# Kernel tuning notes

Hardware: AMD Instinct MI355X
Metric: run time of the kernel (lower is better)

Reference implementation:

```python
import jax, jax.numpy as jnp
import numpy as np


def setup_inputs() -> dict:
    key = jax.random.key(0)
    ks = jax.random.split(key, 6)
    B, Nab, Nag, d, K = 16, 16384, 16384, 128, 10
    return {
        "H1": jax.random.normal(ks[0], (B, Nab, d), jnp.float32),
        "H2": jax.random.normal(ks[1], (B, Nag, d), jnp.float32),
        "X1": jax.random.normal(ks[2], (B, Nab, 3), jnp.float32),
        "X2": jax.random.normal(ks[3], (B, Nag, 3), jnp.float32),
        "W1": jax.random.uniform(ks[4], (K, d, d), jnp.float32),
        "W2": jax.random.uniform(ks[5], (K, d, d), jnp.float32),
    }


def _kabsch(P, Q):
    # Rigid alignment: find R (3x3), t (3,) s.t. P @ R + t ~= Q (least squares).
    c1 = P.mean(axis=0)
    c2 = Q.mean(axis=0)
    Pc = P - c1
    Qc = Q - c2
    Hm = Pc.T @ Qc  # [3,3] covariance
    U, S, Vt = jnp.linalg.svd(Hm, full_matrices=False)
    sign = jnp.sign(jnp.linalg.det(U @ Vt))
    Dm = jnp.diag(jnp.concatenate([jnp.ones(2, dtype=P.dtype), sign[None]]))
    R = U @ Dm @ Vt
    t = c2 - c1 @ R
    return P @ R + t, R, t


def reference(H1, H2, X1, X2, W1, W2):
    # Keypoint cross-attention. Faithful to torch:
    #   alpha_1k = softmax( (H1 @ W1_k @ H2.T).mean(dim=1) / sqrt(d) )
    # Using mean-over-columns identity: (H1 @ W @ H2.T).mean(1) = H1 @ W @ mean(H2,0)
    d = H1.shape[-1]
    scale = 1.0 / np.sqrt(d)
    h2bar = H2.mean(axis=1)  # [B, d]
    h1bar = H1.mean(axis=1)  # [B, d]
    v1 = jnp.einsum('kde,be->bkd', W1, h2bar)          # W1_k @ mean(H2)
    s1 = jnp.einsum('bnd,bkd->bkn', H1, v1) * scale     # [B, K, Nab]
    a1 = jax.nn.softmax(s1, axis=-1)
    Y1 = jnp.einsum('bkn,bnc->bkc', a1, X1)             # [B, K, 3]
    v2 = jnp.einsum('kde,be->bkd', W2, h1bar)
    s2 = jnp.einsum('bmd,bkd->bkm', H2, v2) * scale     # [B, K, Nag]
    a2 = jax.nn.softmax(s2, axis=-1)
    Y2 = jnp.einsum('bkm,bmc->bkc', a2, X2)             # [B, K, 3]
    Y1_aligned, R, t = jax.vmap(_kabsch)(Y1, Y2)
    return jnp.stack([Y1, Y2, Y1_aligned], axis=1)      # [B, 3, K, 3]
```

## Files before the change

### kernel.cpp

```cpp
#include <hip/hip_runtime.h>
#include <math.h>

#define NB 16
#define NN 16384
#define DD 128
#define KK 10

#define WS_FLOATS 46336

__global__ __launch_bounds__(256) void k_means(const float* __restrict__ H1,
                                               const float* __restrict__ H2,
                                               float* __restrict__ hsum) {
    int bi = blockIdx.x;
    int t = bi >> 11;
    int rem = bi & 2047;
    int b = rem >> 7;
    int chunk = rem & 127;
    const float* src = (t ? H2 : H1) + ((size_t)b * NN + (size_t)chunk * 128) * DD;
    const float4* src4 = (const float4*)src;
    int tid = threadIdx.x;

    float4 x[16];
#pragma unroll
    for (int i = 0; i < 16; ++i)
        x[i] = src4[i * 256 + tid];

    float4 s = make_float4(0.f, 0.f, 0.f, 0.f);
#pragma unroll
    for (int i = 0; i < 16; ++i) {
        s.x += x[i].x; s.y += x[i].y; s.z += x[i].z; s.w += x[i].w;
    }
    s.x += __shfl_xor(s.x, 32);
    s.y += __shfl_xor(s.y, 32);
    s.z += __shfl_xor(s.z, 32);
    s.w += __shfl_xor(s.w, 32);
    __shared__ float red[4][32][4];
    int wave = tid >> 6, lane = tid & 63;
    if (lane < 32) {
        red[wave][lane][0] = s.x; red[wave][lane][1] = s.y;
        red[wave][lane][2] = s.z; red[wave][lane][3] = s.w;
    }
    __syncthreads();
    if (tid < 32) {
        float t0 = 0.f, t1 = 0.f, t2 = 0.f, t3 = 0.f;
#pragma unroll
        for (int w = 0; w < 4; ++w) {
            t0 += red[w][tid][0]; t1 += red[w][tid][1];
            t2 += red[w][tid][2]; t3 += red[w][tid][3];
        }
        float* dst = hsum + (size_t)(t * NB + b) * DD + tid * 4;
        atomicAdd(dst + 0, t0);
        atomicAdd(dst + 1, t1);
        atomicAdd(dst + 2, t2);
        atomicAdd(dst + 3, t3);
    }
}

__global__ __launch_bounds__(128) void k_v(const float* __restrict__ W1,
                                           const float* __restrict__ W2,
                                           const float* __restrict__ hsum,
                                           float* __restrict__ v) {
    int bi = blockIdx.x;
    int p = bi / 160;
    int rem = bi % 160;
    int b = rem / 10;
    int k = rem % 10;
    const float* W = (p ? W2 : W1) + (size_t)k * DD * DD;
    const float* hb = hsum + (size_t)((1 - p) * NB + b) * DD;
    __shared__ float4 h_s[32];
    int tid = threadIdx.x;
    if (tid < 32) h_s[tid] = ((const float4*)hb)[tid];
    __syncthreads();
    const float4* Wrow = (const float4*)(W + (size_t)tid * DD);
    float4 w[8];
#pragma unroll
    for (int e = 0; e < 8; ++e) w[e] = Wrow[e];
    float acc = 0.f;
#pragma unroll
    for (int half = 0; half < 4; ++half) {
#pragma unroll
        for (int e = 0; e < 8; ++e) {
            float4 h4 = h_s[half * 8 + e];
            acc += w[e].x * h4.x + w[e].y * h4.y + w[e].z * h4.z + w[e].w * h4.w;
        }
        if (half < 3) {
#pragma unroll
            for (int e = 0; e < 8; ++e) w[e] = Wrow[(half + 1) * 8 + e];
        }
    }
    const float SCALE = (float)(1.0 / (16384.0 * 11.313708498984761));
    v[((size_t)(p * NB + b) * KK + k) * DD + tid] = acc * SCALE;
}

__global__ __launch_bounds__(256) void k_scores(const float* __restrict__ H1,
                                                const float* __restrict__ H2,
                                                const float* __restrict__ X1,
                                                const float* __restrict__ X2,
                                                const float* __restrict__ v,
                                                float* __restrict__ accg) {
    int bi = blockIdx.x;
    int p = bi >> 11;
    int rem = bi & 2047;
    int b = rem >> 7;
    int tile = rem & 127;
    int row0 = tile << 7;
    const float* H = (p ? H2 : H1) + (size_t)b * NN * DD;
    const float* X = (p ? X2 : X1) + (size_t)b * NN * 3;
    const float* vp = v + (size_t)(p * NB + b) * KK * DD;

    __shared__ float4 v_s4[KK * DD / 4];
    __shared__ float red[4][40];
    float* v_s = (float*)v_s4;

    int tid = threadIdx.x;
    for (int i = tid; i < KK * DD / 4; i += 256)
        v_s4[i] = ((const float4*)vp)[i];

    int g = tid >> 3;
    int l = tid & 7;
    int nbase = row0 + (g << 2);

    float4 h[4][4];
#pragma unroll
    for (int j = 0; j < 4; ++j)
#pragma unroll
        for (int r = 0; r < 4; ++r)
            h[j][r] = *(const float4*)(H + (size_t)(nbase + r) * DD + (j << 5) + (l << 2));
    float xv[4][3];
#pragma unroll
    for (int r = 0; r < 4; ++r) {
        const float* xr = X + (size_t)(nbase + r) * 3;
        xv[r][0] = xr[0]; xv[r][1] = xr[1]; xv[r][2] = xr[2];
    }

    __syncthreads();

    float accs[4][KK];
#pragma unroll
    for (int r = 0; r < 4; ++r)
#pragma unroll
        for (int k = 0; k < KK; ++k) accs[r][k] = 0.f;

#pragma unroll
    for (int j = 0; j < 4; ++j) {
#pragma unroll
        for (int k = 0; k < KK; ++k) {
            float4 vv = *(const float4*)(v_s + k * DD + (j << 5) + (l << 2));
#pragma unroll
            for (int r = 0; r < 4; ++r)
                accs[r][k] += h[j][r].x * vv.x + h[j][r].y * vv.y +
                              h[j][r].z * vv.z + h[j][r].w * vv.w;
        }
    }
#pragma unroll
    for (int r = 0; r < 4; ++r)
#pragma unroll
        for (int k = 0; k < KK; ++k) {
            float s = accs[r][k];
            s += __shfl_xor(s, 1);
            s += __shfl_xor(s, 2);
            s += __shfl_xor(s, 4);
            accs[r][k] = s;
        }

    float pSE[KK], pY0[KK], pY1[KK], pY2[KK];
#pragma unroll
    for (int k = 0; k < KK; ++k) { pSE[k] = 0.f; pY0[k] = 0.f; pY1[k] = 0.f; pY2[k] = 0.f; }

#pragma unroll
    for (int r = 0; r < 4; ++r) {
        float x0 = xv[r][0], x1 = xv[r][1], x2 = xv[r][2];
#pragma unroll
        for (int k = 0; k < KK; ++k) {
            float e = __expf(accs[r][k]);
            pSE[k] += e;
            pY0[k] += e * x0;
            pY1[k] += e * x1;
            pY2[k] += e * x2;
        }
    }
#pragma unroll
    for (int k = 0; k < KK; ++k) {
        pSE[k] += __shfl_xor(pSE[k], 8);  pSE[k] += __shfl_xor(pSE[k], 16);  pSE[k] += __shfl_xor(pSE[k], 32);
        pY0[k] += __shfl_xor(pY0[k], 8);  pY0[k] += __shfl_xor(pY0[k], 16);  pY0[k] += __shfl_xor(pY0[k], 32);
        pY1[k] += __shfl_xor(pY1[k], 8);  pY1[k] += __shfl_xor(pY1[k], 16);  pY1[k] += __shfl_xor(pY1[k], 32);
        pY2[k] += __shfl_xor(pY2[k], 8);  pY2[k] += __shfl_xor(pY2[k], 16);  pY2[k] += __shfl_xor(pY2[k], 32);
    }
    int wave = tid >> 6, lane = tid & 63;
    if (lane == 0) {
#pragma unroll
        for (int k = 0; k < KK; ++k) {
            red[wave][k] = pSE[k];
            red[wave][10 + k] = pY0[k];
            red[wave][20 + k] = pY1[k];
            red[wave][30 + k] = pY2[k];
        }
    }
    __syncthreads();
    if (tid < 40) {
        float s = red[0][tid] + red[1][tid] + red[2][tid] + red[3][tid];
        atomicAdd(accg + (size_t)(p * NB + b) * 40 + tid, s);
    }
}

__global__ __launch_bounds__(64) void k_final(const float* __restrict__ accg,
                                              float* __restrict__ out) {
    int b = blockIdx.x;
    int tid = threadIdx.x;
    __shared__ float Ys[2][KK][3];
    if (tid < 2 * KK * 3) {
        int p = tid / 30;
        int r = tid % 30;
        int k = r / 3;
        int c = r % 3;
        const float* a = accg + (size_t)(p * NB + b) * 40;
        float val = a[10 + c * 10 + k] / a[k];
        Ys[p][k][c] = val;
        out[((size_t)(b * 3 + p) * KK + k) * 3 + c] = val;
    }
    __syncthreads();
    if (tid == 0) {
        double P[KK][3], Q[KK][3];
        double c1[3] = {0, 0, 0}, c2[3] = {0, 0, 0};
        for (int i = 0; i < KK; ++i)
            for (int c = 0; c < 3; ++c) {
                P[i][c] = (double)Ys[0][i][c];
                Q[i][c] = (double)Ys[1][i][c];
                c1[c] += P[i][c];
                c2[c] += Q[i][c];
            }
        for (int c = 0; c < 3; ++c) { c1[c] /= KK; c2[c] /= KK; }
        double A0[3][3];
        for (int a = 0; a < 3; ++a)
            for (int c = 0; c < 3; ++c) {
                double s = 0;
                for (int i = 0; i < KK; ++i) s += (P[i][a] - c1[a]) * (Q[i][c] - c2[c]);
                A0[a][c] = s;
            }
        double Bm[3][3], V[3][3];
        for (int a = 0; a < 3; ++a)
            for (int c = 0; c < 3; ++c) { Bm[a][c] = A0[a][c]; V[a][c] = (a == c) ? 1.0 : 0.0; }
        for (int sweep = 0; sweep < 16; ++sweep)
            for (int p = 0; p < 2; ++p)
                for (int q = p + 1; q < 3; ++q) {
                    double al = 0, be = 0, ga = 0;
                    for (int r = 0; r < 3; ++r) {
                        al += Bm[r][p] * Bm[r][p];
                        be += Bm[r][q] * Bm[r][q];
                        ga += Bm[r][p] * Bm[r][q];
                    }
                    if (fabs(ga) < 1e-300) continue;
                    double zeta = (be - al) / (2.0 * ga);
                    double t = copysign(1.0, zeta) / (fabs(zeta) + sqrt(1.0 + zeta * zeta));
                    double cs = 1.0 / sqrt(1.0 + t * t);
                    double sn = cs * t;
                    for (int r = 0; r < 3; ++r) {
                        double bp = Bm[r][p], bq = Bm[r][q];
                        Bm[r][p] = cs * bp - sn * bq;
                        Bm[r][q] = sn * bp + cs * bq;
                        double vp = V[r][p], vq = V[r][q];
                        V[r][p] = cs * vp - sn * vq;
                        V[r][q] = sn * vp + cs * vq;
                    }
                }
        double sig[3];
        for (int j = 0; j < 3; ++j) {
            sig[j] = sqrt(Bm[0][j] * Bm[0][j] + Bm[1][j] * Bm[1][j] + Bm[2][j] * Bm[2][j]);
            if (sig[j] < 1e-300) sig[j] = 1e-300;
        }
        int jmin = 0;
        if (sig[1] < sig[jmin]) jmin = 1;
        if (sig[2] < sig[jmin]) jmin = 2;
        double det = A0[0][0] * (A0[1][1] * A0[2][2] - A0[1][2] * A0[2][1])
                   - A0[0][1] * (A0[1][0] * A0[2][2] - A0[1][2] * A0[2][0])
                   + A0[0][2] * (A0[1][0] * A0[2][1] - A0[1][1] * A0[2][0]);
        double sgn = (det >= 0.0) ? 1.0 : -1.0;
        double R[3][3];
        for (int a = 0; a < 3; ++a)
            for (int c = 0; c < 3; ++c) {
                double s = 0;
                for (int j = 0; j < 3; ++j) {
                    double dj = (j == jmin) ? sgn : 1.0;
                    s += dj * (Bm[a][j] / sig[j]) * V[c][j];
                }
                R[a][c] = s;
            }
        for (int i = 0; i < KK; ++i)
            for (int c = 0; c < 3; ++c) {
                double s = c2[c];
                for (int a = 0; a < 3; ++a) s += (P[i][a] - c1[a]) * R[a][c];
                out[((size_t)(b * 3 + 2) * KK + i) * 3 + c] = (float)s;
            }
    }
}

extern "C" void kernel_launch(void* const* d_in, const int* in_sizes, int n_in,
                              void* d_out, int out_size, void* d_ws, size_t ws_size,
                              hipStream_t stream) {
    const float* H1 = (const float*)d_in[0];
    const float* H2 = (const float*)d_in[1];
    const float* X1 = (const float*)d_in[2];
    const float* X2 = (const float*)d_in[3];
    const float* W1 = (const float*)d_in[4];
    const float* W2 = (const float*)d_in[5];
    float* out = (float*)d_out;
    float* ws = (float*)d_ws;
    float* hsum = ws;
    float* v    = ws + 4096;
    float* accg = ws + 45056;

    hipMemsetAsync(d_ws, 0, WS_FLOATS * sizeof(float), stream);
    hipLaunchKernelGGL(k_means,  dim3(4096), dim3(256), 0, stream, H1, H2, hsum);
    hipLaunchKernelGGL(k_v,      dim3(320),  dim3(128), 0, stream, W1, W2, hsum, v);
    hipLaunchKernelGGL(k_scores, dim3(4096), dim3(256), 0, stream, H1, H2, X1, X2, v, accg);
    hipLaunchKernelGGL(k_final,  dim3(16),   dim3(64),  0, stream, accg, out);
}
```

Measured before the change: 384.7 us.

## Fuse H1 mean into H1 score pass and reorder stages to cut H reads

Rather than reading both H1 and H2 once for means and again for scores, the H2 mean is computed first. The H1 scoring pass then also accumulates the H1 column sums, which feeds the v2 computation before the H2 pass runs. This removes one full read of H1, roughly a quarter of total HBM traffic. It also adds nontemporal loads, a persistent-style grid with 4 tiles per block, and splits k_v and the score pass per side, at the cost of more sequential launches and extra syncs and atomics.

```diff
diff --git a/kernel.cpp b/kernel.cpp
--- a/kernel.cpp
+++ b/kernel.cpp
@@ -8,63 +8,63 @@
 
 #define WS_FLOATS 46336
 
-__global__ __launch_bounds__(256) void k_means(const float* __restrict__ H1,
-                                               const float* __restrict__ H2,
+typedef float f4v __attribute__((ext_vector_type(4)));
+__device__ __forceinline__ float4 ntload4(const float* p) {
+    f4v t = __builtin_nontemporal_load((const f4v*)p);
+    return make_float4(t.x, t.y, t.z, t.w);
+}
+
+__global__ __launch_bounds__(256) void k_mean2(const float* __restrict__ H2,
                                                float* __restrict__ hsum) {
-    int bi = blockIdx.x;
-    int t = bi >> 11;
-    int rem = bi & 2047;
-    int b = rem >> 7;
-    int chunk = rem & 127;
-    const float* src = (t ? H2 : H1) + ((size_t)b * NN + (size_t)chunk * 128) * DD;
-    const float4* src4 = (const float4*)src;
     int tid = threadIdx.x;
-
-    float4 x[16];
-#pragma unroll
-    for (int i = 0; i < 16; ++i)
-        x[i] = src4[i * 256 + tid];
-
-    float4 s = make_float4(0.f, 0.f, 0.f, 0.f);
-#pragma unroll
-    for (int i = 0; i < 16; ++i) {
-        s.x += x[i].x; s.y += x[i].y; s.z += x[i].z; s.w += x[i].w;
-    }
-    s.x += __shfl_xor(s.x, 32);
-    s.y += __shfl_xor(s.y, 32);
-    s.z += __shfl_xor(s.z, 32);
-    s.w += __shfl_xor(s.w, 32);
     __shared__ float red[4][32][4];
-    int wave = tid >> 6, lane = tid & 63;
-    if (lane < 32) {
-        red[wave][lane][0] = s.x; red[wave][lane][1] = s.y;
-        red[wave][lane][2] = s.z; red[wave][lane][3] = s.w;
-    }
-    __syncthreads();
-    if (tid < 32) {
-        float t0 = 0.f, t1 = 0.f, t2 = 0.f, t3 = 0.f;
-#pragma unroll
-        for (int w = 0; w < 4; ++w) {
-            t0 += red[w][tid][0]; t1 += red[w][tid][1];
-            t2 += red[w][tid][2]; t3 += red[w][tid][3];
-        }
-        float* dst = hsum + (size_t)(t * NB + b) * DD + tid * 4;
-        atomicAdd(dst + 0, t0);
-        atomicAdd(dst + 1, t1);
-        atomicAdd(dst + 2, t2);
-        atomicAdd(dst + 3, t3);
+    for (int it = 0; it < 2; ++it) {
+        int tau = blockIdx.x + it * 1024;
+        int b = tau >> 7;
+        const float4* src4 = (const float4*)(H2 + (size_t)tau * (128 * DD));
+        float4 x[16];
+#pragma unroll
+        for (int i = 0; i < 16; ++i)
+            x[i] = src4[i * 256 + tid];
+        float4 s = make_float4(0.f, 0.f, 0.f, 0.f);
+#pragma unroll
+        for (int i = 0; i < 16; ++i) {
+            s.x += x[i].x; s.y += x[i].y; s.z += x[i].z; s.w += x[i].w;
+        }
+        s.x += __shfl_xor(s.x, 32);
+        s.y += __shfl_xor(s.y, 32);
+        s.z += __shfl_xor(s.z, 32);
+        s.w += __shfl_xor(s.w, 32);
+        int wave = tid >> 6, lane = tid & 63;
+        if (lane < 32) {
+            red[wave][lane][0] = s.x; red[wave][lane][1] = s.y;
+            red[wave][lane][2] = s.z; red[wave][lane][3] = s.w;
+        }
+        __syncthreads();
+        if (tid < 32) {
+            float t0 = 0.f, t1 = 0.f, t2 = 0.f, t3 = 0.f;
+#pragma unroll
+            for (int w = 0; w < 4; ++w) {
+                t0 += red[w][tid][0]; t1 += red[w][tid][1];
+                t2 += red[w][tid][2]; t3 += red[w][tid][3];
+            }
+            float* dst = hsum + (size_t)(NB + b) * DD + tid * 4;
+            atomicAdd(dst + 0, t0);
+            atomicAdd(dst + 1, t1);
+            atomicAdd(dst + 2, t2);
+            atomicAdd(dst + 3, t3);
+        }
+        __syncthreads();
     }
 }
 
 __global__ __launch_bounds__(128) void k_v(const float* __restrict__ W1,
                                            const float* __restrict__ W2,
                                            const float* __restrict__ hsum,
-                                           float* __restrict__ v) {
+                                           float* __restrict__ v, int p) {
     int bi = blockIdx.x;
-    int p = bi / 160;
-    int rem = bi % 160;
-    int b = rem / 10;
-    int k = rem % 10;
+    int b = bi / 10;
+    int k = bi % 10;
     const float* W = (p ? W2 : W1) + (size_t)k * DD * DD;
     const float* hb = hsum + (size_t)((1 - p) * NB + b) * DD;
     __shared__ float4 h_s[32];
@@ -72,134 +72,155 @@
     if (tid < 32) h_s[tid] = ((const float4*)hb)[tid];
     __syncthreads();
     const float4* Wrow = (const float4*)(W + (size_t)tid * DD);
-    float4 w[8];
-#pragma unroll
-    for (int e = 0; e < 8; ++e) w[e] = Wrow[e];
     float acc = 0.f;
-#pragma unroll
-    for (int half = 0; half < 4; ++half) {
-#pragma unroll
-        for (int e = 0; e < 8; ++e) {
-            float4 h4 = h_s[half * 8 + e];
-            acc += w[e].x * h4.x + w[e].y * h4.y + w[e].z * h4.z + w[e].w * h4.w;
-        }
-        if (half < 3) {
-#pragma unroll
-            for (int e = 0; e < 8; ++e) w[e] = Wrow[(half + 1) * 8 + e];
-        }
+#pragma unroll 8
+    for (int e4 = 0; e4 < 32; ++e4) {
+        float4 w4 = Wrow[e4];
+        float4 h4 = h_s[e4];
+        acc += w4.x * h4.x + w4.y * h4.y + w4.z * h4.z + w4.w * h4.w;
     }
     const float SCALE = (float)(1.0 / (16384.0 * 11.313708498984761));
     v[((size_t)(p * NB + b) * KK + k) * DD + tid] = acc * SCALE;
 }
 
-__global__ __launch_bounds__(256) void k_scores(const float* __restrict__ H1,
-                                                const float* __restrict__ H2,
-                                                const float* __restrict__ X1,
-                                                const float* __restrict__ X2,
-                                                const float* __restrict__ v,
-                                                float* __restrict__ accg) {
-    int bi = blockIdx.x;
-    int p = bi >> 11;
-    int rem = bi & 2047;
-    int b = rem >> 7;
-    int tile = rem & 127;
-    int row0 = tile << 7;
-    const float* H = (p ? H2 : H1) + (size_t)b * NN * DD;
-    const float* X = (p ? X2 : X1) + (size_t)b * NN * 3;
-    const float* vp = v + (size_t)(p * NB + b) * KK * DD;
-
+__global__ __launch_bounds__(256) void k_pass(const float* __restrict__ H,
+                                              const float* __restrict__ X,
+                                              const float* __restrict__ v,
+                                              float* __restrict__ accg,
+                                              float* __restrict__ hsumout,
+                                              int do_sum) {
     __shared__ float4 v_s4[KK * DD / 4];
     __shared__ float red[4][40];
+    __shared__ float4 sred[4][4][8];
     float* v_s = (float*)v_s4;
 
     int tid = threadIdx.x;
-    for (int i = tid; i < KK * DD / 4; i += 256)
-        v_s4[i] = ((const float4*)vp)[i];
-
     int g = tid >> 3;
     int l = tid & 7;
-    int nbase = row0 + (g << 2);
-
-    float4 h[4][4];
-#pragma unroll
-    for (int j = 0; j < 4; ++j)
+
+    for (int it = 0; it < 4; ++it) {
+        int tau = blockIdx.x + it * 512;
+        int b = tau >> 7;
+        const float* Hb = H + (size_t)tau * (128 * DD);
+        const float* Xb = X + ((size_t)b * NN + (size_t)(tau & 127) * 128) * 3;
+        const float* vp = v + (size_t)b * KK * DD;
+        int nb = g << 2;
+
+        float4 h[4][4];
+#pragma unroll
+        for (int j = 0; j < 4; ++j)
+#pragma unroll
+            for (int r = 0; r < 4; ++r)
+                h[j][r] = ntload4(Hb + (size_t)(nb + r) * DD + (j << 5) + (l << 2));
+        float xv[4][3];
+#pragma unroll
+        for (int r = 0; r < 4; ++r) {
+            const float* xr = Xb + (size_t)(nb + r) * 3;
+            xv[r][0] = xr[0]; xv[r][1] = xr[1]; xv[r][2] = xr[2];
+        }
+
+        __syncthreads();
+        for (int i = tid; i < KK * DD / 4; i += 256)
+            v_s4[i] = ((const float4*)vp)[i];
+        __syncthreads();
+
+        float accs[4][KK];
 #pragma unroll
         for (int r = 0; r < 4; ++r)
-            h[j][r] = *(const float4*)(H + (size_t)(nbase + r) * DD + (j << 5) + (l << 2));
-    float xv[4][3];
-#pragma unroll
-    for (int r = 0; r < 4; ++r) {
-        const float* xr = X + (size_t)(nbase + r) * 3;
-        xv[r][0] = xr[0]; xv[r][1] = xr[1]; xv[r][2] = xr[2];
-    }
-
-    __syncthreads();
-
-    float accs[4][KK];
-#pragma unroll
-    for (int r = 0; r < 4; ++r)
-#pragma unroll
-        for (int k = 0; k < KK; ++k) accs[r][k] = 0.f;
-
-#pragma unroll
-    for (int j = 0; j < 4; ++j) {
+#pragma unroll
+            for (int k = 0; k < KK; ++k) accs[r][k] = 0.f;
+
+#pragma unroll
+        for (int j = 0; j < 4; ++j) {
+#pragma unroll
+            for (int k = 0; k < KK; ++k) {
+                float4 vv = *(const float4*)(v_s + k * DD + (j << 5) + (l << 2));
+#pragma unroll
+                for (int r = 0; r < 4; ++r)
+                    accs[r][k] += h[j][r].x * vv.x + h[j][r].y * vv.y +
+                                  h[j][r].z * vv.z + h[j][r].w * vv.w;
+            }
+        }
+#pragma unroll
+        for (int r = 0; r < 4; ++r)
+#pragma unroll
+            for (int k = 0; k < KK; ++k) {
+                float s = accs[r][k];
+                s += __shfl_xor(s, 1);
+                s += __shfl_xor(s, 2);
+                s += __shfl_xor(s, 4);
+                accs[r][k] = s;
+            }
+
+        float pSE[KK], pY0[KK], pY1[KK], pY2[KK];
+#pragma unroll
+        for (int k = 0; k < KK; ++k) { pSE[k] = 0.f; pY0[k] = 0.f; pY1[k] = 0.f; pY2[k] = 0.f; }
+
+#pragma unroll
+        for (int r = 0; r < 4; ++r) {
+            float x0 = xv[r][0], x1 = xv[r][1], x2 = xv[r][2];
+#pragma unroll
+            for (int k = 0; k < KK; ++k) {
+                float e = __expf(accs[r][k]);
+                pSE[k] += e;
+                pY0[k] += e * x0;
+                pY1[k] += e * x1;
+                pY2[k] += e * x2;
+            }
+        }
 #pragma unroll
         for (int k = 0; k < KK; ++k) {
-            float4 vv = *(const float4*)(v_s + k * DD + (j << 5) + (l << 2));
-#pragma unroll
-            for (int r = 0; r < 4; ++r)
-                accs[r][k] += h[j][r].x * vv.x + h[j][r].y * vv.y +
-                              h[j][r].z * vv.z + h[j][r].w * vv.w;
-        }
-    }
-#pragma unroll
-    for (int r = 0; r < 4; ++r)
-#pragma unroll
-        for (int k = 0; k < KK; ++k) {
-            float s = accs[r][k];
-            s += __shfl_xor(s, 1);
-            s += __shfl_xor(s, 2);
-            s += __shfl_xor(s, 4);
-            accs[r][k] = s;
-        }
-
-    float pSE[KK], pY0[KK], pY1[KK], pY2[KK];
-#pragma unroll
-    for (int k = 0; k < KK; ++k) { pSE[k] = 0.f; pY0[k] = 0.f; pY1[k] = 0.f; pY2[k] = 0.f; }
-
-#pragma unroll
-    for (int r = 0; r < 4; ++r) {
-        float x0 = xv[r][0], x1 = xv[r][1], x2 = xv[r][2];
-#pragma unroll
-        for (int k = 0; k < KK; ++k) {
-            float e = __expf(accs[r][k]);
-            pSE[k] += e;
-            pY0[k] += e * x0;
-            pY1[k] += e * x1;
-            pY2[k] += e * x2;
-        }
-    }
-#pragma unroll
-    for (int k = 0; k < KK; ++k) {
-        pSE[k] += __shfl_xor(pSE[k], 8);  pSE[k] += __shfl_xor(pSE[k], 16);  pSE[k] += __shfl_xor(pSE[k], 32);
-        pY0[k] += __shfl_xor(pY0[k], 8);  pY0[k] += __shfl_xor(pY0[k], 16);  pY0[k] += __shfl_xor(pY0[k], 32);
-        pY1[k] += __shfl_xor(pY1[k], 8);  pY1[k] += __shfl_xor(pY1[k], 16);  pY1[k] += __shfl_xor(pY1[k], 32);
-        pY2[k] += __shfl_xor(pY2[k], 8);  pY2[k] += __shfl_xor(pY2[k], 16);  pY2[k] += __shfl_xor(pY2[k], 32);
-    }
-    int wave = tid >> 6, lane = tid & 63;
-    if (lane == 0) {
-#pragma unroll
-        for (int k = 0; k < KK; ++k) {
-            red[wave][k] = pSE[k];
-            red[wave][10 + k] = pY0[k];
-            red[wave][20 + k] = pY1[k];
-            red[wave][30 + k] = pY2[k];
-        }
-    }
-    __syncthreads();
-    if (tid < 40) {
-        float s = red[0][tid] + red[1][tid] + red[2][tid] + red[3][tid];
-        atomicAdd(accg + (size_t)(p * NB + b) * 40 + tid, s);
+            pSE[k] += __shfl_xor(pSE[k], 8);  pSE[k] += __shfl_xor(pSE[k], 16);  pSE[k] += __shfl_xor(pSE[k], 32);
+            pY0[k] += __shfl_xor(pY0[k], 8);  pY0[k] += __shfl_xor(pY0[k], 16);  pY0[k] += __shfl_xor(pY0[k], 32);
+            pY1[k] += __shfl_xor(pY1[k], 8);  pY1[k] += __shfl_xor(pY1[k], 16);  pY1[k] += __shfl_xor(pY1[k], 32);
+            pY2[k] += __shfl_xor(pY2[k], 8);  pY2[k] += __shfl_xor(pY2[k], 16);  pY2[k] += __shfl_xor(pY2[k], 32);
+        }
+        int wave = tid >> 6, lane = tid & 63;
+        if (lane == 0) {
+#pragma unroll
+            for (int k = 0; k < KK; ++k) {
+                red[wave][k] = pSE[k];
+                red[wave][10 + k] = pY0[k];
+                red[wave][20 + k] = pY1[k];
+                red[wave][30 + k] = pY2[k];
+            }
+        }
+        if (do_sum) {
+            float4 cs[4];
+#pragma unroll
+            for (int j = 0; j < 4; ++j) {
+                cs[j].x = h[j][0].x + h[j][1].x + h[j][2].x + h[j][3].x;
+                cs[j].y = h[j][0].y + h[j][1].y + h[j][2].y + h[j][3].y;
+                cs[j].z = h[j][0].z + h[j][1].z + h[j][2].z + h[j][3].z;
+                cs[j].w = h[j][0].w + h[j][1].w + h[j][2].w + h[j][3].w;
+            }
+#pragma unroll
+            for (int j = 0; j < 4; ++j) {
+                cs[j].x += __shfl_xor(cs[j].x, 8); cs[j].x += __shfl_xor(cs[j].x, 16); cs[j].x += __shfl_xor(cs[j].x, 32);
+                cs[j].y += __shfl_xor(cs[j].y, 8); cs[j].y += __shfl_xor(cs[j].y, 16); cs[j].y += __shfl_xor(cs[j].y, 32);
+                cs[j].z += __shfl_xor(cs[j].z, 8); cs[j].z += __shfl_xor(cs[j].z, 16); cs[j].z += __shfl_xor(cs[j].z, 32);
+                cs[j].w += __shfl_xor(cs[j].w, 8); cs[j].w += __shfl_xor(cs[j].w, 16); cs[j].w += __shfl_xor(cs[j].w, 32);
+            }
+            if (lane < 8) {
+#pragma unroll
+                for (int j = 0; j < 4; ++j) sred[wave][j][lane] = cs[j];
+            }
+        }
+        __syncthreads();
+        if (tid < 40) {
+            float s = red[0][tid] + red[1][tid] + red[2][tid] + red[3][tid];
+            atomicAdd(accg + (size_t)b * 40 + tid, s);
+        }
+        if (do_sum && tid >= 64 && tid < 96) {
+            int t2 = tid - 64;
+            int j = t2 >> 3, l2 = t2 & 7;
+            float4 a0 = sred[0][j][l2], a1 = sred[1][j][l2], a2 = sred[2][j][l2], a3 = sred[3][j][l2];
+            float* dst = hsumout + (size_t)b * DD + (j << 5) + (l2 << 2);
+            atomicAdd(dst + 0, a0.x + a1.x + a2.x + a3.x);
+            atomicAdd(dst + 1, a0.y + a1.y + a2.y + a3.y);
+            atomicAdd(dst + 2, a0.z + a1.z + a2.z + a3.z);
+            atomicAdd(dst + 3, a0.w + a1.w + a2.w + a3.w);
+        }
     }
 }
 
@@ -310,8 +331,12 @@
     float* accg = ws + 45056;
 
     hipMemsetAsync(d_ws, 0, WS_FLOATS * sizeof(float), stream);
-    hipLaunchKernelGGL(k_means,  dim3(4096), dim3(256), 0, stream, H1, H2, hsum);
-    hipLaunchKernelGGL(k_v,      dim3(320),  dim3(128), 0, stream, W1, W2, hsum, v);
-    hipLaunchKernelGGL(k_scores, dim3(4096), dim3(256), 0, stream, H1, H2, X1, X2, v, accg);
-    hipLaunchKernelGGL(k_final,  dim3(16),   dim3(64),  0, stream, accg, out);
-}
+    hipLaunchKernelGGL(k_mean2, dim3(1024), dim3(256), 0, stream, H2, hsum);
+    hipLaunchKernelGGL(k_v, dim3(160), dim3(128), 0, stream, W1, W2, hsum, v, 0);
+    hipLaunchKernelGGL(k_pass, dim3(512), dim3(256), 0, stream,
+                       H1, X1, v, accg, hsum, 1);
+    hipLaunchKernelGGL(k_v, dim3(160), dim3(128), 0, stream, W1, W2, hsum, v, 1);
+    hipLaunchKernelGGL(k_pass, dim3(512), dim3(256), 0, stream,
+                       H2, X2, v + (size_t)NB * KK * DD, accg + (size_t)NB * 40, hsum, 0);
+    hipLaunchKernelGGL(k_final, dim3(16), dim3(64), 0, stream, accg, out);
+}
```

Result: slower. 401.2 us (+4.3%).
